# Optimization experiments

Measured on AMD Instinct MI355X. Metric: run time of the kernel, lower is better.

Reference implementation:

```python
import jax, jax.numpy as jnp
import numpy as np

V, N, K, D = 2, 100000, 8, 128
TAU = 1.0
LOG_2PI = float(np.log(2.0 * np.pi))


def setup_inputs() -> dict:
    key = jax.random.key(0)
    k1, k2, k3 = jax.random.split(key, 3)
    z = jax.random.normal(k1, (V, N, D), dtype=jnp.float32)
    phi = jnp.ones((V, K), dtype=jnp.float32) / K
    mu = jax.random.normal(k2, (V, K, D), dtype=jnp.float32)
    # sigma: identity (as in torch init) plus a small symmetric PSD perturbation
    a = 0.05 * jax.random.normal(k3, (V, K, D, D), dtype=jnp.float32)
    sigma = jnp.eye(D, dtype=jnp.float32) + jnp.einsum('vkde,vkfe->vkdf', a, a)
    return {"z": z, "phi": phi, "mu": mu, "sigma": sigma}


def _compute_energy(z, phi, mu, sigma):
    # z: [N, D]; phi: [K]; mu: [K, D]; sigma: [K, D, D]
    eps_eye = 1e-6 * jnp.eye(D, dtype=z.dtype)
    sigma_stable = sigma + eps_eye  # [K, D, D]
    inv_sigma = jnp.linalg.inv(sigma_stable)
    det_sigma = jnp.clip(jnp.linalg.det(sigma_stable), 1e-6, None)  # [K]
    diff = z[:, None, :] - mu[None, :, :]  # [N, K, D]
    maha = jnp.einsum('nkd,kde,nke->nk', diff, inv_sigma, diff)  # [N, K]
    log_pi = jax.nn.log_softmax(phi)  # [K]
    log_prob = (-0.5 * maha
                - 0.5 * D * LOG_2PI
                - 0.5 * jnp.log(det_sigma)[None, :]
                + log_pi[None, :])  # [N, K]
    energy = -jax.nn.logsumexp(log_prob, axis=1)  # [N]
    penalty = jnp.sum(1.0 / (jnp.diagonal(sigma_stable, axis1=-2, axis2=-1) + 1e-12))
    return energy, penalty


def reference(z, phi, mu, sigma):
    # vmap over views; energies_v: [V, N]
    energies_v, penalties = jax.vmap(_compute_energy)(z, phi, mu, sigma)
    energies = energies_v.T  # [N, V]
    total_energies = jnp.sum(energies)
    total_penalty = jnp.sum(penalties)
    weights = jax.nn.softmax(-energies / TAU, axis=1)  # [N, V]
    return energies, weights, total_energies, total_penalty
```

## Files before the change

kernel.cpp:

```cpp
#include <hip/hip_runtime.h>
#include <math.h>

#define V 2
#define NN 100000
#define KK 8
#define DD 128
#define TILE_N 128
#define SL 132
#define NT 782
#define CH 8
#define CPX 13
#define NPAD 100096
#define LOG2PI 1.8378770664093454f
#define LOG_1EM6 -13.815510557964274f

#define IMG_B 69632
#define IMG_HALF 17408
#define LF_B   1114112
#define BV_B   2228224
#define C_B    2236416
#define MAHA_B 2236480

#define OUT_W_OFF (NN*V)
#define OUT_TE (2*NN*V)
#define OUT_TP (2*NN*V + 1)

typedef __attribute__((ext_vector_type(8))) short bf16x8;
typedef __attribute__((ext_vector_type(4))) float f32x4;
typedef __attribute__((ext_vector_type(4))) unsigned u32x4;

__device__ __forceinline__ unsigned short f2bf_rtn(float f) {
    unsigned u = __builtin_bit_cast(unsigned, f);
    unsigned r = u + 0x7FFFu + ((u >> 16) & 1u);
    return (unsigned short)(r >> 16);
}
__device__ __forceinline__ float bf2f(unsigned short h) {
    unsigned u = ((unsigned)h) << 16;
    return __builtin_bit_cast(float, u);
}

__device__ __forceinline__ void cvt_pair(float f0, float f1, unsigned& hi, unsigned& lo) {
    unsigned u0 = __builtin_bit_cast(unsigned, f0);
    unsigned u1 = __builtin_bit_cast(unsigned, f1);
    hi = __builtin_amdgcn_perm(u1, u0, 0x07060302u);
    float r0 = f0 - __builtin_bit_cast(float, u0 & 0xFFFF0000u);
    float r1 = f1 - __builtin_bit_cast(float, u1 & 0xFFFF0000u);
    unsigned v0 = __builtin_bit_cast(unsigned, r0) + 0x8000u;
    unsigned v1 = __builtin_bit_cast(unsigned, r1) + 0x8000u;
    lo = __builtin_amdgcn_perm(v1, v0, 0x07060302u);
}

__global__ void zero_kernel(float* out) {
    int t = threadIdx.x;
    if (t < 2) out[OUT_TE + t] = 0.0f;
}

__global__ __launch_bounds__(256) void prep_chol(const float* __restrict__ phi,
                                                 const float* __restrict__ mu,
                                                 const float* __restrict__ sigma,
                                                 void* __restrict__ wsv,
                                                 float* __restrict__ out) {
    __shared__ float Lf[DD * SL];
    __shared__ float P[8][SL];
    __shared__ float dvec[DD];
    __shared__ float mulds[DD];
    __shared__ float red[256];
    __shared__ float Bv[8];
    __shared__ float Bb[DD];

    const int tid = threadIdx.x;
    const int vk  = blockIdx.x;
    const int v   = vk >> 3;
    const int k   = vk & 7;
    const int R   = tid >> 4;
    const int C   = tid & 15;

    if (tid < DD) mulds[tid] = mu[vk * DD + tid];

    float A[8][8];
    const float* sig = sigma + (size_t)vk * DD * DD;
    float pen = 0.0f;
    #pragma unroll
    for (int a = 0; a < 8; ++a) {
        const float4* p4 = (const float4*)(sig + (size_t)(8 * R + a) * DD + 8 * C);
        float4 x = p4[0], y = p4[1];
        A[a][0] = x.x; A[a][1] = x.y; A[a][2] = x.z; A[a][3] = x.w;
        A[a][4] = y.x; A[a][5] = y.y; A[a][6] = y.z; A[a][7] = y.w;
        if (R == C) A[a][a] += 1e-6f;
    }
    if (R == C) {
        #pragma unroll
        for (int a = 0; a < 8; ++a) pen += 1.0f / (A[a][a] + 1e-12f);
    }

    for (int i = tid; i < DD * SL; i += 256) Lf[i] = 0.0f;

    red[tid] = pen;
    __syncthreads();
    for (int s = 128; s > 0; s >>= 1) {
        if (tid < s) red[tid] += red[tid + s];
        __syncthreads();
    }
    if (tid == 0) atomicAdd(&out[OUT_TP], red[0]);
    __syncthreads();

    for (int p = 0; p < 16; ++p) {
        if (C == p && R >= p) {
            #pragma unroll
            for (int b = 0; b < 8; ++b) {
                *(float4*)&P[b][8 * R]     = make_float4(A[0][b], A[1][b], A[2][b], A[3][b]);
                *(float4*)&P[b][8 * R + 4] = make_float4(A[4][b], A[5][b], A[6][b], A[7][b]);
            }
        }
        __syncthreads();

        if (tid < 64) {
            const int lane = tid;
            const int r1 = 8 * p + lane;
            const int r2 = r1 + 64;
            const bool ok2 = (r2 < DD);
            float pr1[8], pr2[8], rs[8];
            #pragma unroll
            for (int j = 0; j < 8; ++j) {
                pr1[j] = (r1 < DD) ? P[j][r1] : 0.0f;
                pr2[j] = ok2 ? P[j][r2] : 0.0f;
            }
            #pragma unroll
            for (int j = 0; j < 8; ++j) {
                if (lane >= j && lane < 8) Bv[lane] = pr1[j];
                __builtin_amdgcn_wave_barrier();
                float bv[8];
                #pragma unroll
                for (int m = 0; m < 8; ++m) bv[m] = Bv[m];
                __builtin_amdgcn_wave_barrier();
                float piv = bv[j];
                if (lane == j) dvec[8 * p + j] = piv;
                float inv2 = 1.0f / piv;
                rs[j] = rsqrtf(piv);
                float m1 = pr1[j] * inv2;
                float m2 = pr2[j] * inv2;
                #pragma unroll
                for (int j2 = 0; j2 < 8; ++j2) {
                    if (j2 > j) {
                        if (lane > j) pr1[j2] -= m1 * bv[j2];
                        pr2[j2] -= m2 * bv[j2];
                    }
                }
            }
            #pragma unroll
            for (int j = 0; j < 8; ++j) {
                if (r1 < DD) {
                    float v1 = (lane >= j) ? pr1[j] * rs[j] : 0.0f;
                    P[j][r1] = v1;
                    Lf[r1 * SL + 8 * p + j] = v1;
                }
                if (ok2) {
                    float v2 = pr2[j] * rs[j];
                    P[j][r2] = v2;
                    Lf[r2 * SL + 8 * p + j] = v2;
                }
            }
        }
        __syncthreads();

        if (C > p && R >= p) {
            #pragma unroll
            for (int j = 0; j < 8; ++j) {
                float4 a0 = *(const float4*)&P[j][8 * R];
                float4 a1 = *(const float4*)&P[j][8 * R + 4];
                float4 b0 = *(const float4*)&P[j][8 * C];
                float4 b1 = *(const float4*)&P[j][8 * C + 4];
                float ra[8] = {a0.x, a0.y, a0.z, a0.w, a1.x, a1.y, a1.z, a1.w};
                float rb[8] = {b0.x, b0.y, b0.z, b0.w, b1.x, b1.y, b1.z, b1.w};
                #pragma unroll
                for (int a = 0; a < 8; ++a)
                    #pragma unroll
                    for (int b = 0; b < 8; ++b)
                        A[a][b] -= ra[a] * rb[b];
            }
        }
        __syncthreads();
    }

    if (tid < 64) {
        const int lane = tid;
        float acc0 = mulds[lane];
        float acc1 = mulds[lane + 64];
        for (int j = 0; j < DD; ++j) {
            if (j < 64) { if (lane == j)      Bb[j] = acc0 / Lf[j * SL + j]; }
            else        { if (lane == j - 64) Bb[j] = acc1 / Lf[j * SL + j]; }
            __builtin_amdgcn_wave_barrier();
            float bj = Bb[j];
            __builtin_amdgcn_wave_barrier();
            if (lane > j)      acc0 -= Lf[lane * SL + j] * bj;
            if (lane + 64 > j) acc1 -= Lf[(lane + 64) * SL + j] * bj;
        }
    }
    __syncthreads();
    if (tid < DD) ((float*)((char*)wsv + BV_B))[vk * DD + tid] = Bb[tid];

    {
        float4* Lg = (float4*)((char*)wsv + LF_B + (size_t)vk * IMG_B);
        const float4* Ls4 = (const float4*)Lf;
        for (int i = tid; i < DD * SL / 4; i += 256) Lg[i] = Ls4[i];
    }

    red[tid] = (tid < DD) ? logf(dvec[tid]) : 0.0f;
    __syncthreads();
    for (int s = 128; s > 0; s >>= 1) {
        if (tid < s) red[tid] += red[tid + s];
        __syncthreads();
    }
    if (tid == 0) {
        float logdet_c = fmaxf(red[0], LOG_1EM6);
        const float* ph = phi + v * KK;
        float m = ph[0];
        for (int i = 1; i < KK; ++i) m = fmaxf(m, ph[i]);
        float s = 0.0f;
        for (int i = 0; i < KK; ++i) s += expf(ph[i] - m);
        float logpi = ph[k] - m - logf(s);
        ((float*)((char*)wsv + C_B))[vk] = logpi - 0.5f * logdet_c - 0.5f * (float)DD * LOG2PI;
    }
}

__global__ __launch_bounds__(256) void prep_trsm(void* __restrict__ wsv) {
    __shared__ float Ls[DD * SL];
    __shared__ float Wc[32][SL];

    const int tid = threadIdx.x;
    const int vk  = blockIdx.x >> 2;
    const int cg  = blockIdx.x & 3;

    const float4* Lg = (const float4*)((const char*)wsv + LF_B + (size_t)vk * IMG_B);
    float4* Ls4 = (float4*)Ls;
    for (int i = tid; i < DD * SL / 4; i += 256) Ls4[i] = Lg[i];
    __syncthreads();

    const int c   = tid >> 3;
    const int par = tid & 7;
    const int j   = 4 * c + cg;

    for (int e = par; e < SL; e += 8) Wc[c][e] = 0.0f;
    if (par == 0) Wc[c][j] = 1.0f / Ls[j * SL + j];
    __builtin_amdgcn_wave_barrier();

    const int pbase = j & ~3;
    for (int i = j + 1; i < DD; ++i) {
        float s = 0.0f;
        for (int p4 = pbase + 4 * par; p4 < i; p4 += 32) {
            float4 lf = *(const float4*)&Ls[i * SL + p4];
            float4 wc = *(const float4*)&Wc[c][p4];
            s += lf.x * wc.x + lf.y * wc.y + lf.z * wc.z + lf.w * wc.w;
        }
        s += __shfl_xor(s, 1, 64);
        s += __shfl_xor(s, 2, 64);
        s += __shfl_xor(s, 4, 64);
        if (par == 0) Wc[c][i] = -s / Ls[i * SL + i];
        __builtin_amdgcn_wave_barrier();
    }

    unsigned short* Gh = (unsigned short*)((char*)wsv + (size_t)vk * IMG_B);
    unsigned short* Gl = Gh + IMG_HALF;
    for (int i2 = par; i2 < DD; i2 += 8) {
        float f = (i2 >= j) ? Wc[c][i2] : 0.0f;
        unsigned short h = f2bf_rtn(f);
        unsigned short l = f2bf_rtn(f - bf2f(h));
        Gh[i2 * 136 + j] = h;
        Gl[i2 * 136 + j] = l;
    }
}

__global__ __launch_bounds__(256, 2) void maha_kernel(const float* __restrict__ z,
                                                      void* __restrict__ wsv) {
    __shared__ unsigned short wl[IMG_B / 2];
    __shared__ float bl_s[DD];

    const int tid  = threadIdx.x;
    const int lane = tid & 63;
    const int wave = tid >> 6;
    const int quad = lane >> 4;
    const int l16  = lane & 15;

    const int bi    = blockIdx.x;
    const int xcd   = bi & 7;
    const int jj    = bi >> 3;
    const int r     = jj & 15;
    const int lc    = jj >> 4;
    const int chunk = xcd * CPX + lc;
    const int vv    = r >> 3;

    if (chunk * CH >= NT) return;

    {
        const char* src = (const char*)wsv + (size_t)r * IMG_B;
        char* dst = (char*)wl;
        const int lane_off = wave * 1024 + lane * 16;
        #pragma unroll
        for (int t = 0; t < 17; ++t)
            __builtin_amdgcn_global_load_lds(
                (const __attribute__((address_space(1))) void*)(src + t * 4096 + lane_off),
                (__attribute__((address_space(3))) void*)(dst + t * 4096 + wave * 1024),
                16, 0, 0);
    }
    if (tid < DD) bl_s[tid] = ((const float*)((const char*)wsv + BV_B))[r * DD + tid];
    __syncthreads();

    const float* zbase = z + (size_t)vv * NN * DD;
    float* mrow = (float*)((char*)wsv + MAHA_B) + (size_t)r * NPAD;

    float4 pre[2][4][2];

    auto load_tile = [&](int tt) {
        #pragma unroll
        for (int mt = 0; mt < 2; ++mt) {
            const int n = tt * TILE_N + wave * 32 + mt * 16 + l16;
            const bool ok = (n < NN);
            const float* zp = zbase + (size_t)n * DD + quad * 8;
            #pragma unroll
            for (int ds = 0; ds < 4; ++ds) {
                if (ok) {
                    pre[mt][ds][0] = *(const float4*)(zp + ds * 32);
                    pre[mt][ds][1] = *(const float4*)(zp + ds * 32 + 4);
                } else {
                    pre[mt][ds][0] = make_float4(0.f, 0.f, 0.f, 0.f);
                    pre[mt][ds][1] = make_float4(0.f, 0.f, 0.f, 0.f);
                }
            }
        }
    };

    load_tile(chunk * CH);

    for (int ti = 0; ti < CH; ++ti) {
        const int t = chunk * CH + ti;
        if (t >= NT) break;
        const int n0 = t * TILE_N;

        u32x4 zh[2][4], zl[2][4];
        #pragma unroll
        for (int mt = 0; mt < 2; ++mt)
            #pragma unroll
            for (int ds = 0; ds < 4; ++ds) {
                float4 a = pre[mt][ds][0];
                float4 b = pre[mt][ds][1];
                unsigned h0, l0, h1, l1, h2, l2, h3, l3;
                cvt_pair(a.x, a.y, h0, l0);
                cvt_pair(a.z, a.w, h1, l1);
                cvt_pair(b.x, b.y, h2, l2);
                cvt_pair(b.z, b.w, h3, l3);
                u32x4 th, tl;
                th[0] = h0; th[1] = h1; th[2] = h2; th[3] = h3;
                tl[0] = l0; tl[1] = l1; tl[2] = l2; tl[3] = l3;
                zh[mt][ds] = th;
                zl[mt][ds] = tl;
            }

        if (ti + 1 < CH && t + 1 < NT) load_tile(t + 1);

        f32x4 acc[2][8];
        #pragma unroll
        for (int mt = 0; mt < 2; ++mt)
            #pragma unroll
            for (int nt = 0; nt < 8; ++nt)
                acc[mt][nt] = (f32x4)(0.0f);

        #pragma unroll
        for (int ds = 0; ds < 4; ++ds) {
            const int g = ds * 4 + quad;
            #pragma unroll
            for (int nt = 2 * ds; nt < 8; ++nt) {
                const int row = nt * 16 + l16;
                const int off = row * 136 + g * 8;
                bf16x8 bh  = *(const bf16x8*)&wl[off];
                bf16x8 blo = *(const bf16x8*)&wl[IMG_HALF + off];
                #pragma unroll
                for (int mt = 0; mt < 2; ++mt) {
                    bf16x8 ah = __builtin_bit_cast(bf16x8, zh[mt][ds]);
                    bf16x8 al = __builtin_bit_cast(bf16x8, zl[mt][ds]);
                    acc[mt][nt] = __builtin_amdgcn_mfma_f32_16x16x32_bf16(ah, bh,  acc[mt][nt], 0, 0, 0);
                    acc[mt][nt] = __builtin_amdgcn_mfma_f32_16x16x32_bf16(ah, blo, acc[mt][nt], 0, 0, 0);
                    acc[mt][nt] = __builtin_amdgcn_mfma_f32_16x16x32_bf16(al, bh,  acc[mt][nt], 0, 0, 0);
                }
            }
        }

        #pragma unroll
        for (int mt = 0; mt < 2; ++mt) {
            float p[4] = {0.f, 0.f, 0.f, 0.f};
            #pragma unroll
            for (int nt = 0; nt < 8; ++nt) {
                float bc = bl_s[nt * 16 + l16];
                f32x4 a = acc[mt][nt];
                float y0 = a[0] - bc, y1 = a[1] - bc, y2 = a[2] - bc, y3 = a[3] - bc;
                p[0] += y0 * y0; p[1] += y1 * y1; p[2] += y2 * y2; p[3] += y3 * y3;
            }
            float sv[4];
            #pragma unroll
            for (int reg = 0; reg < 4; ++reg) {
                float s = p[reg];
                s += __shfl_xor(s, 1, 64);
                s += __shfl_xor(s, 2, 64);
                s += __shfl_xor(s, 4, 64);
                s += __shfl_xor(s, 8, 64);
                sv[reg] = s;
            }
            if (l16 == 0)
                *(float4*)&mrow[n0 + wave * 32 + mt * 16 + quad * 4] =
                    make_float4(sv[0], sv[1], sv[2], sv[3]);
        }
    }
}

__global__ __launch_bounds__(256) void finalize_kernel(const void* __restrict__ wsv,
                                                       float* __restrict__ out) {
    __shared__ float red[256];
    __shared__ float clds[16];

    const int tid = threadIdx.x;
    if (tid < 16) clds[tid] = ((const float*)((const char*)wsv + C_B))[tid];
    __syncthreads();

    const float* mahap = (const float*)((const char*)wsv + MAHA_B);
    const int n = blockIdx.x * 256 + tid;
    float esum = 0.0f;

    if (n < NN) {
        float ev[V];
        #pragma unroll
        for (int vv = 0; vv < V; ++vv) {
            float lp[KK];
            float m = -1e30f;
            #pragma unroll
            for (int k = 0; k < KK; ++k) {
                int r = vv * KK + k;
                lp[k] = -0.5f * mahap[(size_t)r * NPAD + n] + clds[r];
                m = fmaxf(m, lp[k]);
            }
            float s = 0.0f;
            #pragma unroll
            for (int k = 0; k < KK; ++k) s += expf(lp[k] - m);
            ev[vv] = -(m + logf(s));
        }
        float e0 = ev[0], e1 = ev[1];
        float m = fmaxf(-e0, -e1);
        float x0 = expf(-e0 - m);
        float x1 = expf(-e1 - m);
        float inv = 1.0f / (x0 + x1);
        out[(size_t)n * V + 0] = e0;
        out[(size_t)n * V + 1] = e1;
        out[OUT_W_OFF + (size_t)n * V + 0] = x0 * inv;
        out[OUT_W_OFF + (size_t)n * V + 1] = x1 * inv;
        esum = e0 + e1;
    }

    red[tid] = esum;
    __syncthreads();
    for (int s = 128; s > 0; s >>= 1) {
        if (tid < s) red[tid] += red[tid + s];
        __syncthreads();
    }
    if (tid == 0) atomicAdd(&out[OUT_TE], red[0]);
}

extern "C" void kernel_launch(void* const* d_in, const int* in_sizes, int n_in,
                              void* d_out, int out_size, void* d_ws, size_t ws_size,
                              hipStream_t stream) {
    const float* z     = (const float*)d_in[0];
    const float* phi   = (const float*)d_in[1];
    const float* mu    = (const float*)d_in[2];
    const float* sigma = (const float*)d_in[3];
    float* out = (float*)d_out;

    hipLaunchKernelGGL(zero_kernel, dim3(1), dim3(64), 0, stream, out);
    hipLaunchKernelGGL(prep_chol, dim3(V * KK), dim3(256), 0, stream, phi, mu, sigma, d_ws, out);
    hipLaunchKernelGGL(prep_trsm, dim3(64), dim3(256), 0, stream, d_ws);
    hipLaunchKernelGGL(maha_kernel, dim3(8 * CPX * 16), dim3(256), 0, stream, z, d_ws);
    hipLaunchKernelGGL(finalize_kernel, dim3((NPAD + 255) / 256), dim3(256), 0, stream, d_ws, out);
}
```

Measured before the change: 393.6 us.

## Pack triangular whitening matrix in LDS and fold bias into accumulator init

The bf16 hi/lo whitening image is stored in a packed block-triangular layout (40 KB instead of 68 KB), so the maha kernel stages less data into LDS and its launch bound rises from 2 to 4 blocks per CU for more occupancy. The per-column bias is moved from LDS into registers and used as the MFMA accumulator's initial value, which removes a subtraction from the epilogue. The packed indexing adds address arithmetic, and the higher block count per CU tightens the register budget, which may cause spills.

After: 850.7 us. 2.16x slower.

```diff
diff --git a/kernel.cpp b/kernel.cpp
--- a/kernel.cpp
+++ b/kernel.cpp
@@ -14,9 +14,11 @@
 #define LOG2PI 1.8378770664093454f
 #define LOG_1EM6 -13.815510557964274f
 
-#define IMG_B 69632
-#define IMG_HALF 17408
+#define IMG_PB 40960
+#define IMG_LO_US 10240
+
 #define LF_B   1114112
+#define LF_STRIDE 69632
 #define BV_B   2228224
 #define C_B    2236416
 #define MAHA_B 2236480
@@ -200,7 +202,7 @@
     if (tid < DD) ((float*)((char*)wsv + BV_B))[vk * DD + tid] = Bb[tid];
 
     {
-        float4* Lg = (float4*)((char*)wsv + LF_B + (size_t)vk * IMG_B);
+        float4* Lg = (float4*)((char*)wsv + LF_B + (size_t)vk * LF_STRIDE);
         const float4* Ls4 = (const float4*)Lf;
         for (int i = tid; i < DD * SL / 4; i += 256) Lg[i] = Ls4[i];
     }
@@ -231,7 +233,7 @@
     const int vk  = blockIdx.x >> 2;
     const int cg  = blockIdx.x & 3;
 
-    const float4* Lg = (const float4*)((const char*)wsv + LF_B + (size_t)vk * IMG_B);
+    const float4* Lg = (const float4*)((const char*)wsv + LF_B + (size_t)vk * LF_STRIDE);
     float4* Ls4 = (float4*)Ls;
     for (int i = tid; i < DD * SL / 4; i += 256) Ls4[i] = Lg[i];
     __syncthreads();
@@ -259,21 +261,24 @@
         __builtin_amdgcn_wave_barrier();
     }
 
-    unsigned short* Gh = (unsigned short*)((char*)wsv + (size_t)vk * IMG_B);
-    unsigned short* Gl = Gh + IMG_HALF;
+    unsigned short* Gh = (unsigned short*)((char*)wsv + (size_t)vk * IMG_PB);
+    const int HBUS[4] = {0, 1024, 3072, 6144};
     for (int i2 = par; i2 < DD; i2 += 8) {
+        const int b = i2 >> 5;
+        if ((j >> 5) > b) continue;
+        const int ri  = i2 & 31;
+        const int off = HBUS[b] + ri * 32 * (b + 1) + j;
         float f = (i2 >= j) ? Wc[c][i2] : 0.0f;
         unsigned short h = f2bf_rtn(f);
         unsigned short l = f2bf_rtn(f - bf2f(h));
-        Gh[i2 * 136 + j] = h;
-        Gl[i2 * 136 + j] = l;
-    }
-}
-
-__global__ __launch_bounds__(256, 2) void maha_kernel(const float* __restrict__ z,
+        Gh[off] = h;
+        Gh[off + IMG_LO_US] = l;
+    }
+}
+
+__global__ __launch_bounds__(256, 4) void maha_kernel(const float* __restrict__ z,
                                                       void* __restrict__ wsv) {
-    __shared__ unsigned short wl[IMG_B / 2];
-    __shared__ float bl_s[DD];
+    __shared__ unsigned short wl[IMG_PB / 2];
 
     const int tid  = threadIdx.x;
     const int lane = tid & 63;
@@ -292,17 +297,23 @@
     if (chunk * CH >= NT) return;
 
     {
-        const char* src = (const char*)wsv + (size_t)r * IMG_B;
+        const char* src = (const char*)wsv + (size_t)r * IMG_PB;
         char* dst = (char*)wl;
         const int lane_off = wave * 1024 + lane * 16;
         #pragma unroll
-        for (int t = 0; t < 17; ++t)
+        for (int t = 0; t < 10; ++t)
             __builtin_amdgcn_global_load_lds(
                 (const __attribute__((address_space(1))) void*)(src + t * 4096 + lane_off),
                 (__attribute__((address_space(3))) void*)(dst + t * 4096 + wave * 1024),
                 16, 0, 0);
     }
-    if (tid < DD) bl_s[tid] = ((const float*)((const char*)wsv + BV_B))[r * DD + tid];
+
+    float blr[8];
+    {
+        const float* bvp = (const float*)((const char*)wsv + BV_B) + r * DD;
+        #pragma unroll
+        for (int nt = 0; nt < 8; ++nt) blr[nt] = bvp[nt * 16 + l16];
+    }
     __syncthreads();
 
     const float* zbase = z + (size_t)vv * NN * DD;
@@ -362,17 +373,19 @@
         for (int mt = 0; mt < 2; ++mt)
             #pragma unroll
             for (int nt = 0; nt < 8; ++nt)
-                acc[mt][nt] = (f32x4)(0.0f);
+                acc[mt][nt] = (f32x4)(-blr[nt]);
 
         #pragma unroll
         for (int ds = 0; ds < 4; ++ds) {
             const int g = ds * 4 + quad;
             #pragma unroll
             for (int nt = 2 * ds; nt < 8; ++nt) {
-                const int row = nt * 16 + l16;
-                const int off = row * 136 + g * 8;
+                const int b   = nt >> 1;
+                const int ri  = ((nt & 1) << 4) + l16;
+                const int off = (b == 0 ? 0 : b == 1 ? 1024 : b == 2 ? 3072 : 6144)
+                                + ri * 32 * (b + 1) + g * 8;
                 bf16x8 bh  = *(const bf16x8*)&wl[off];
-                bf16x8 blo = *(const bf16x8*)&wl[IMG_HALF + off];
+                bf16x8 blo = *(const bf16x8*)&wl[off + IMG_LO_US];
                 #pragma unroll
                 for (int mt = 0; mt < 2; ++mt) {
                     bf16x8 ah = __builtin_bit_cast(bf16x8, zh[mt][ds]);
@@ -389,10 +402,9 @@
             float p[4] = {0.f, 0.f, 0.f, 0.f};
             #pragma unroll
             for (int nt = 0; nt < 8; ++nt) {
-                float bc = bl_s[nt * 16 + l16];
                 f32x4 a = acc[mt][nt];
-                float y0 = a[0] - bc, y1 = a[1] - bc, y2 = a[2] - bc, y3 = a[3] - bc;
-                p[0] += y0 * y0; p[1] += y1 * y1; p[2] += y2 * y2; p[3] += y3 * y3;
+                p[0] += a[0] * a[0]; p[1] += a[1] * a[1];
+                p[2] += a[2] * a[2]; p[3] += a[3] * a[3];
             }
             float sv[4];
             #pragma unroll
```
